# Optimization experiments

Measured on AMD Instinct MI355X. Metric: run time of the kernel, lower is better.

## Reference

```python
import jax, jax.numpy as jnp
import numpy as np

TAU = 0.2
EPS = 1e-12  # torch F.normalize eps

def _l2norm(x):
    n = jnp.sqrt(jnp.sum(x * x, axis=-1, keepdims=True))
    return x / jnp.maximum(n, EPS)

def setup_inputs() -> dict:
    key = jax.random.key(0)
    k1, k2 = jax.random.split(key)
    B, Nx, Ny, D = 2, 8192, 8192, 128
    feat_x = jax.random.normal(k1, (B, Nx, D), dtype=jnp.float32)
    feat_y = jax.random.normal(k2, (B, Ny, D), dtype=jnp.float32)
    verts_mask_x = jnp.ones((B, Nx), dtype=jnp.float32)
    verts_mask_y = jnp.ones((B, Ny), dtype=jnp.float32)
    return {"feat_x": feat_x, "feat_y": feat_y, "verts_mask_x": verts_mask_x, "verts_mask_y": verts_mask_y}

def reference(feat_x, feat_y, verts_mask_x, verts_mask_y):
    # cosine similarity scores: [B, Nx, Ny]
    log_alpha = jnp.einsum('bxd,byd->bxy', _l2norm(feat_x), _l2norm(feat_y)) / TAU
    # stable softmax over last dim (normalise_dim = -1)
    alpha = jax.nn.softmax(log_alpha, axis=-1)
    # double masking: rows by mask_x, cols by mask_y
    return alpha * verts_mask_x[:, :, None] * verts_mask_y[:, None, :]
```

## Files before the change

### kernel.cpp

```cpp
#include <hip/hip_runtime.h>
#include <hip/hip_bf16.h>


typedef __attribute__((ext_vector_type(8))) short short8;
typedef __attribute__((ext_vector_type(4))) float float4v;

constexpr int B = 2, NX = 8192, NY = 8192, DD = 128;
constexpr int BM = 128, BN = 128;
constexpr int NSPLIT = 8;
constexpr int YCHUNK = NY / NSPLIT;
constexpr int ROWB = 256;
constexpr float TAU_INV = 5.0f;

__device__ __forceinline__ void gload16(const void* g, void* l) {
    __builtin_amdgcn_global_load_lds(
        (const __attribute__((address_space(1))) void*)g,
        (__attribute__((address_space(3))) void*)l, 16, 0, 0);
}

__device__ __forceinline__ void stage_tile(const char* gsrc, char* lds, int wid, int lane) {
    const int srow = wid * 32;
    const int lr4 = lane >> 4;
    const int lcb = (lane & 15) * 16;
#pragma unroll
    for (int i = 0; i < 8; ++i) {
        int row = srow + i * 4 + lr4;
        int scb = lcb ^ ((row & 7) << 4);
        gload16(gsrc + (size_t)row * ROWB + scb, lds + (srow + i * 4) * ROWB);
    }
}

__global__ __launch_bounds__(256) void l2norm_kernel(const float* __restrict__ in,
                                                     __hip_bfloat16* __restrict__ out,
                                                     int rows) {
    int wid = threadIdx.x >> 6, lane = threadIdx.x & 63;
    int row = blockIdx.x * 4 + wid;
    if (row >= rows) return;
    float2 v = ((const float2*)(in + (size_t)row * DD))[lane];
    float ss = v.x * v.x + v.y * v.y;
#pragma unroll
    for (int off = 32; off >= 1; off >>= 1) ss += __shfl_xor(ss, off);
    float inv = 1.0f / fmaxf(sqrtf(ss), 1e-12f);
    __hip_bfloat162 o;
    o.x = __float2bfloat16(v.x * inv);
    o.y = __float2bfloat16(v.y * inv);
    ((__hip_bfloat162*)(out + (size_t)row * DD))[lane] = o;
}

__global__ __launch_bounds__(256) void pass1_kernel(const __hip_bfloat16* __restrict__ Xn,
                                                    const __hip_bfloat16* __restrict__ Yn,
                                                    float* __restrict__ partial) {
    __shared__ __hip_bfloat16 Xs[BM][DD];
    __shared__ __hip_bfloat16 Ys[BN][DD];
    const int split = blockIdx.x, xt = blockIdx.y, b = blockIdx.z;
    const int t = threadIdx.x;
    const int lane = t & 63, wid = t >> 6;
    const int wm = wid >> 1, wn = wid & 1;
    const int lrow = lane & 15, lhi = lane >> 4;

    stage_tile((const char*)(Xn + (size_t)(b * NX + xt * BM) * DD), (char*)&Xs[0][0], wid, lane);

    float run[4][4];
#pragma unroll
    for (int m = 0; m < 4; ++m)
#pragma unroll
        for (int r = 0; r < 4; ++r) run[m][r] = 0.f;

    for (int tile = 0; tile < YCHUNK / BN; ++tile) {
        __syncthreads();
        stage_tile((const char*)(Yn + (size_t)(b * NY + split * YCHUNK + tile * BN) * DD),
                   (char*)&Ys[0][0], wid, lane);
        __syncthreads();

        float4v acc[4][4];
#pragma unroll
        for (int m = 0; m < 4; ++m)
#pragma unroll
            for (int n = 0; n < 4; ++n) acc[m][n] = (float4v)(0.f);
#pragma unroll
        for (int kk = 0; kk < 4; ++kk) {
            const int cb = (kk * 64 + lhi * 16) ^ ((lrow & 7) << 4);
            short8 a[4], bb[4];
#pragma unroll
            for (int m = 0; m < 4; ++m)
                a[m] = *(const short8*)((const char*)Xs + (size_t)(wm * 64 + m * 16 + lrow) * ROWB + cb);
#pragma unroll
            for (int n = 0; n < 4; ++n)
                bb[n] = *(const short8*)((const char*)Ys + (size_t)(wn * 64 + n * 16 + lrow) * ROWB + cb);
#pragma unroll
            for (int m = 0; m < 4; ++m)
#pragma unroll
                for (int n = 0; n < 4; ++n)
                    acc[m][n] = __builtin_amdgcn_mfma_f32_16x16x32_bf16(a[m], bb[n], acc[m][n], 0, 0, 0);
        }
#pragma unroll
        for (int m = 0; m < 4; ++m)
#pragma unroll
            for (int r = 0; r < 4; ++r) {
                float s = 0.f;
#pragma unroll
                for (int n = 0; n < 4; ++n) s += __expf(acc[m][n][r] * TAU_INV);
                run[m][r] += s;
            }
    }

#pragma unroll
    for (int m = 0; m < 4; ++m)
#pragma unroll
        for (int r = 0; r < 4; ++r) {
            float v = run[m][r];
            v += __shfl_xor(v, 1);
            v += __shfl_xor(v, 2);
            v += __shfl_xor(v, 4);
            v += __shfl_xor(v, 8);
            run[m][r] = v;
        }

    __syncthreads();
    float* lred = (float*)Ys;
    if (lrow == 0) {
#pragma unroll
        for (int m = 0; m < 4; ++m)
#pragma unroll
            for (int r = 0; r < 4; ++r) {
                int xl = wm * 64 + m * 16 + lhi * 4 + r;
                lred[wn * BM + xl] = run[m][r];
            }
    }
    __syncthreads();
    if (t < BM) {
        float tot = lred[t] + lred[BM + t];
        partial[(size_t)split * (B * NX) + (size_t)b * NX + xt * BM + t] = tot;
    }
}

__global__ void combine_kernel(const float* __restrict__ partial,
                               const float* __restrict__ maskx,
                               float* __restrict__ rowscale) {
    int idx = blockIdx.x * 256 + threadIdx.x;
    if (idx >= B * NX) return;
    float s = 0.f;
#pragma unroll
    for (int i = 0; i < NSPLIT; ++i) s += partial[(size_t)i * (B * NX) + idx];
    rowscale[idx] = maskx[idx] / s;
}

__global__ __launch_bounds__(256) void pass2_kernel(const __hip_bfloat16* __restrict__ Xn,
                                                    const __hip_bfloat16* __restrict__ Yn,
                                                    const float* __restrict__ rowscale,
                                                    const float* __restrict__ masky,
                                                    float* __restrict__ out) {
    __shared__ __hip_bfloat16 Xs[BM][DD];
    __shared__ __hip_bfloat16 Ys[BN][DD];
    const int yt = blockIdx.x, xt = blockIdx.y, b = blockIdx.z;
    const int t = threadIdx.x;
    const int lane = t & 63, wid = t >> 6;
    const int wy = wid >> 1, wx = wid & 1;
    const int lrow = lane & 15, lhi = lane >> 4;

    stage_tile((const char*)(Xn + (size_t)(b * NX + xt * BM) * DD), (char*)&Xs[0][0], wid, lane);
    stage_tile((const char*)(Yn + (size_t)(b * NY + yt * BN) * DD), (char*)&Ys[0][0], wid, lane);
    __syncthreads();

    float4v acc[4][4];
#pragma unroll
    for (int n = 0; n < 4; ++n)
#pragma unroll
        for (int m = 0; m < 4; ++m) acc[n][m] = (float4v)(0.f);

#pragma unroll
    for (int kk = 0; kk < 4; ++kk) {
        const int cb = (kk * 64 + lhi * 16) ^ ((lrow & 7) << 4);
        short8 a[4], bb[4];
#pragma unroll
        for (int n = 0; n < 4; ++n)
            a[n] = *(const short8*)((const char*)Ys + (size_t)(wy * 64 + n * 16 + lrow) * ROWB + cb);
#pragma unroll
        for (int m = 0; m < 4; ++m)
            bb[m] = *(const short8*)((const char*)Xs + (size_t)(wx * 64 + m * 16 + lrow) * ROWB + cb);
#pragma unroll
        for (int n = 0; n < 4; ++n)
#pragma unroll
            for (int m = 0; m < 4; ++m)
                acc[n][m] = __builtin_amdgcn_mfma_f32_16x16x32_bf16(a[n], bb[m], acc[n][m], 0, 0, 0);
    }

    const int ybase = yt * BN + wy * 64;
    const int xbase = xt * BM + wx * 64;

    float rs[4];
#pragma unroll
    for (int m = 0; m < 4; ++m)
        rs[m] = rowscale[(size_t)b * NX + xbase + m * 16 + lrow];
    float4v my4[4];
#pragma unroll
    for (int n = 0; n < 4; ++n)
        my4[n] = *(const float4v*)(masky + (size_t)b * NY + ybase + n * 16 + lhi * 4);

#pragma unroll
    for (int m = 0; m < 4; ++m) {
        const int x = xbase + m * 16 + lrow;
        float* orow = out + ((size_t)b * NX + x) * NY;
#pragma unroll
        for (int n = 0; n < 4; ++n) {
            float4v o;
#pragma unroll
            for (int r = 0; r < 4; ++r)
                o[r] = __expf(acc[n][m][r] * TAU_INV) * rs[m] * my4[n][r];
            *(float4v*)(orow + ybase + n * 16 + lhi * 4) = o;
        }
    }
}

extern "C" void kernel_launch(void* const* d_in, const int* in_sizes, int n_in,
                              void* d_out, int out_size, void* d_ws, size_t ws_size,
                              hipStream_t stream) {
    const float* feat_x = (const float*)d_in[0];
    const float* feat_y = (const float*)d_in[1];
    const float* maskx  = (const float*)d_in[2];
    const float* masky  = (const float*)d_in[3];
    float* out = (float*)d_out;

    char* ws = (char*)d_ws;
    __hip_bfloat16* Xn = (__hip_bfloat16*)ws;
    __hip_bfloat16* Yn = (__hip_bfloat16*)(ws + (size_t)B * NX * DD * 2);
    float* partial  = (float*)(ws + (size_t)B * (NX + NY) * DD * 2);
    float* rowscale = partial + (size_t)NSPLIT * B * NX;

    l2norm_kernel<<<B * NX / 4, 256, 0, stream>>>(feat_x, Xn, B * NX);
    l2norm_kernel<<<B * NY / 4, 256, 0, stream>>>(feat_y, Yn, B * NY);
    pass1_kernel<<<dim3(NSPLIT, NX / BM, B), 256, 0, stream>>>(Xn, Yn, partial);
    combine_kernel<<<(B * NX + 255) / 256, 256, 0, stream>>>(partial, maskx, rowscale);
    pass2_kernel<<<dim3(NY / BN, NX / BM, B), 256, 0, stream>>>(Xn, Yn, rowscale, masky, out);
}
```

Measured before the change: 178.5 us.

## Double-buffer Y tiles in pass1 to overlap loads with MFMA

Pass1 now splits each Y chunk into 64-row tiles held in two LDS buffers. It prefetches the next tile with async global-to-LDS loads while the current tile is multiplied, which cuts the barriers per iteration from two to one. The aim is to hide global load latency during the row-sum pass. The trade-off is that smaller tiles halve the reuse of each loaded A fragment, so more LDS reads are needed per MFMA. The staging helper is also generalised to take a row count as a template parameter.

```diff
diff --git a/kernel.cpp b/kernel.cpp
--- a/kernel.cpp
+++ b/kernel.cpp
@@ -7,8 +7,10 @@
 
 constexpr int B = 2, NX = 8192, NY = 8192, DD = 128;
 constexpr int BM = 128, BN = 128;
+constexpr int BN1 = 64;
 constexpr int NSPLIT = 8;
 constexpr int YCHUNK = NY / NSPLIT;
+constexpr int NT1 = YCHUNK / BN1;
 constexpr int ROWB = 256;
 constexpr float TAU_INV = 5.0f;
 
@@ -18,15 +20,17 @@
         (__attribute__((address_space(3))) void*)l, 16, 0, 0);
 }
 
-__device__ __forceinline__ void stage_tile(const char* gsrc, char* lds, int wid, int lane) {
-    const int srow = wid * 32;
+template<int NR>
+__device__ __forceinline__ void stage_rows(const char* gsrc, char* lds, int wid, int lane) {
+    constexpr int RPW = NR / 4;
+    const int srow = wid * RPW;
     const int lr4 = lane >> 4;
     const int lcb = (lane & 15) * 16;
 #pragma unroll
-    for (int i = 0; i < 8; ++i) {
-        int row = srow + i * 4 + lr4;
+    for (int i = 0; i < RPW; i += 4) {
+        int row = srow + i + lr4;
         int scb = lcb ^ ((row & 7) << 4);
-        gload16(gsrc + (size_t)row * ROWB + scb, lds + (srow + i * 4) * ROWB);
+        gload16(gsrc + (size_t)row * ROWB + scb, lds + (size_t)(srow + i) * ROWB);
     }
 }
 
@@ -51,14 +55,18 @@
                                                     const __hip_bfloat16* __restrict__ Yn,
                                                     float* __restrict__ partial) {
     __shared__ __hip_bfloat16 Xs[BM][DD];
-    __shared__ __hip_bfloat16 Ys[BN][DD];
+    __shared__ __hip_bfloat16 Ys[2][BN1][DD];
     const int split = blockIdx.x, xt = blockIdx.y, b = blockIdx.z;
     const int t = threadIdx.x;
     const int lane = t & 63, wid = t >> 6;
     const int wm = wid >> 1, wn = wid & 1;
     const int lrow = lane & 15, lhi = lane >> 4;
 
-    stage_tile((const char*)(Xn + (size_t)(b * NX + xt * BM) * DD), (char*)&Xs[0][0], wid, lane);
+    const char* gy0 = (const char*)(Yn + (size_t)(b * NY + split * YCHUNK) * DD);
+
+    stage_rows<BM>((const char*)(Xn + (size_t)(b * NX + xt * BM) * DD), (char*)&Xs[0][0], wid, lane);
+    stage_rows<BN1>(gy0, (char*)&Ys[0][0][0], wid, lane);
+    __syncthreads();
 
     float run[4][4];
 #pragma unroll
@@ -66,31 +74,31 @@
 #pragma unroll
         for (int r = 0; r < 4; ++r) run[m][r] = 0.f;
 
-    for (int tile = 0; tile < YCHUNK / BN; ++tile) {
-        __syncthreads();
-        stage_tile((const char*)(Yn + (size_t)(b * NY + split * YCHUNK + tile * BN) * DD),
-                   (char*)&Ys[0][0], wid, lane);
-        __syncthreads();
-
-        float4v acc[4][4];
-#pragma unroll
-        for (int m = 0; m < 4; ++m)
-#pragma unroll
-            for (int n = 0; n < 4; ++n) acc[m][n] = (float4v)(0.f);
+    for (int tile = 0; tile < NT1; ++tile) {
+        const int cur = tile & 1;
+        if (tile + 1 < NT1)
+            stage_rows<BN1>(gy0 + (size_t)(tile + 1) * BN1 * ROWB,
+                            (char*)&Ys[cur ^ 1][0][0], wid, lane);
+
+        float4v acc[4][2];
+#pragma unroll
+        for (int m = 0; m < 4; ++m)
+#pragma unroll
+            for (int n = 0; n < 2; ++n) acc[m][n] = (float4v)(0.f);
 #pragma unroll
         for (int kk = 0; kk < 4; ++kk) {
             const int cb = (kk * 64 + lhi * 16) ^ ((lrow & 7) << 4);
-            short8 a[4], bb[4];
+            short8 a[4], bb[2];
 #pragma unroll
             for (int m = 0; m < 4; ++m)
                 a[m] = *(const short8*)((const char*)Xs + (size_t)(wm * 64 + m * 16 + lrow) * ROWB + cb);
 #pragma unroll
-            for (int n = 0; n < 4; ++n)
-                bb[n] = *(const short8*)((const char*)Ys + (size_t)(wn * 64 + n * 16 + lrow) * ROWB + cb);
+            for (int n = 0; n < 2; ++n)
+                bb[n] = *(const short8*)((const char*)Ys[cur] + (size_t)(wn * 32 + n * 16 + lrow) * ROWB + cb);
 #pragma unroll
             for (int m = 0; m < 4; ++m)
 #pragma unroll
-                for (int n = 0; n < 4; ++n)
+                for (int n = 0; n < 2; ++n)
                     acc[m][n] = __builtin_amdgcn_mfma_f32_16x16x32_bf16(a[m], bb[n], acc[m][n], 0, 0, 0);
         }
 #pragma unroll
@@ -99,9 +107,10 @@
             for (int r = 0; r < 4; ++r) {
                 float s = 0.f;
 #pragma unroll
-                for (int n = 0; n < 4; ++n) s += __expf(acc[m][n][r] * TAU_INV);
+                for (int n = 0; n < 2; ++n) s += __expf(acc[m][n][r] * TAU_INV);
                 run[m][r] += s;
             }
+        __syncthreads();
     }
 
 #pragma unroll
@@ -116,8 +125,7 @@
             run[m][r] = v;
         }
 
-    __syncthreads();
-    float* lred = (float*)Ys;
+    float* lred = (float*)Xs;
     if (lrow == 0) {
 #pragma unroll
         for (int m = 0; m < 4; ++m)
@@ -158,8 +166,8 @@
     const int wy = wid >> 1, wx = wid & 1;
     const int lrow = lane & 15, lhi = lane >> 4;
 
-    stage_tile((const char*)(Xn + (size_t)(b * NX + xt * BM) * DD), (char*)&Xs[0][0], wid, lane);
-    stage_tile((const char*)(Yn + (size_t)(b * NY + yt * BN) * DD), (char*)&Ys[0][0], wid, lane);
+    stage_rows<BM>((const char*)(Xn + (size_t)(b * NX + xt * BM) * DD), (char*)&Xs[0][0], wid, lane);
+    stage_rows<BN>((const char*)(Yn + (size_t)(b * NY + yt * BN) * DD), (char*)&Ys[0][0], wid, lane);
     __syncthreads();
 
     float4v acc[4][4];
```

New measurement: 187.9 us. 1.05x slower.
